# Kernel optimization log

Hardware: AMD Instinct MI355X
Metric: run time of the kernel (lower is better)

## Reference

```python
import jax, jax.numpy as jnp
import numpy as np

KH = KW = 3
STRIDE = 1
PAD = 1
DIL = 1


def _bilinear_sample(img, py, px):
    Hin, Win = img.shape[-2], img.shape[-1]
    y0 = jnp.floor(py)
    x0 = jnp.floor(px)
    y0i = y0.astype(jnp.int32)
    x0i = x0.astype(jnp.int32)
    wy = py - y0
    wx = px - x0

    def get(yi, xi):
        valid = (yi >= 0) & (yi < Hin) & (xi >= 0) & (xi < Win)
        yc = jnp.clip(yi, 0, Hin - 1)
        xc = jnp.clip(xi, 0, Win - 1)
        v = img[:, yc, xc]  # [C, K, H, W]
        return v * valid[None].astype(img.dtype)

    v00 = get(y0i, x0i)
    v01 = get(y0i, x0i + 1)
    v10 = get(y0i + 1, x0i)
    v11 = get(y0i + 1, x0i + 1)
    return (v00 * (1 - wy) * (1 - wx) + v01 * (1 - wy) * wx
            + v10 * wy * (1 - wx) + v11 * wy * wx)  # [C, K, H, W]


def _deform_conv(input, offset, mask, weight, bias):
    B, C, H, W = input.shape
    outH = (H + 2 * PAD - DIL * (KH - 1) - 1) // STRIDE + 1
    outW = (W + 2 * PAD - DIL * (KW - 1) - 1) // STRIDE + 1
    K = KH * KW
    # NOTE: DepthOffset in the original source overwrites its computed
    # depth-guided offsets with zeros and detaches them, so the effective
    # sampling offset is just `offset` (standard modulated deform conv, DCNv2).
    off = offset.reshape(B, K, 2, outH, outW)
    off_y = off[:, :, 0]  # [B, K, outH, outW]
    off_x = off[:, :, 1]
    ky = (jnp.arange(K) // KW) * DIL  # kernel-tap row offsets
    kx = (jnp.arange(K) % KW) * DIL
    ys = jnp.arange(outH) * STRIDE - PAD
    xs = jnp.arange(outW) * STRIDE - PAD
    base_y = (ky[:, None, None] + ys[None, :, None]).astype(input.dtype)  # [K, outH, 1]
    base_x = (kx[:, None, None] + xs[None, None, :]).astype(input.dtype)  # [K, 1, outW]
    py = base_y[None] + off_y  # [B, K, outH, outW]
    px = base_x[None] + off_x
    cols = jax.vmap(_bilinear_sample)(input, py, px)  # [B, C, K, outH, outW]
    cols = cols * mask[:, None]  # modulate by mask [B, 1, K, outH, outW]
    out = jnp.einsum('bckhw,ock->bohw', cols, weight.reshape(weight.shape[0], C, K))
    return out + bias[None, :, None, None]


def setup_inputs() -> dict:
    key = jax.random.key(0)
    ks = jax.random.split(key, 6)
    B, C, H, W = 4, 64, 128, 128
    O = 64
    fan_in = C * KH * KW
    bound = 1.0 / np.sqrt(fan_in)
    return {
        'input': jax.random.normal(ks[0], (B, C, H, W), dtype=jnp.float32),
        'depth': jax.random.uniform(ks[1], (B, 1, H, W), dtype=jnp.float32),
        'offset': jax.random.normal(ks[2], (B, 18, H, W), dtype=jnp.float32),
        'mask': jax.random.uniform(ks[3], (B, 9, H, W), dtype=jnp.float32),
        'weight': jax.random.uniform(ks[4], (O, C, KH, KW), dtype=jnp.float32,
                                     minval=-bound, maxval=bound),
        'bias': jax.random.uniform(ks[5], (O,), dtype=jnp.float32,
                                   minval=-bound, maxval=bound),
    }


def reference(input, depth, offset, mask, weight, bias):
    # depth-guided offsets are computed then zeroed+detached in the original
    # module, so depth does not influence the output.
    return _deform_conv(input, offset, mask, weight, bias)
```

## Files before the change

### kernel.cpp

```cpp
#include <hip/hip_runtime.h>


typedef __attribute__((ext_vector_type(8))) short bf16x8;
typedef __attribute__((ext_vector_type(4))) float f32x4;
typedef __attribute__((ext_vector_type(2))) float f32x2;
typedef __attribute__((ext_vector_type(4))) unsigned int u32x4;

#define HH 128
#define WW 128
#define CC 64
#define OO 64
#define HW (128 * 128)

__device__ __forceinline__ unsigned f32_to_bf16_rne(float f) {
    unsigned u = __float_as_uint(f);
    return (u + 0x7FFFu + ((u >> 16) & 1u)) >> 16;
}

__global__ __launch_bounds__(256)
void prep_fused15(const float* __restrict__ input,
                  unsigned short* __restrict__ nhwc,
                  const float* __restrict__ weight,
                  unsigned short* __restrict__ wT2)
{
    __shared__ unsigned tile[64][33];
    const int tid = threadIdx.x;
    const int blk = blockIdx.x;

    if (blk >= 2048) {
        const int d  = (blk - 2048) * 256 + tid;
        const int o  = d & 63;
        const int k8 = d >> 6;
        const int kt = k8 >> 3;
        const int c8 = k8 & 7;
        u32x4 pk;
        #pragma unroll
        for (int jj = 0; jj < 4; ++jj) {
            unsigned lo = f32_to_bf16_rne(weight[o * 576 + (c8 * 8 + 2 * jj)     * 9 + kt]);
            unsigned hi = f32_to_bf16_rne(weight[o * 576 + (c8 * 8 + 2 * jj + 1) * 9 + kt]);
            pk[jj] = lo | (hi << 16);
        }
        *(u32x4*)(wT2 + (size_t)d * 8) = pk;
        return;
    }

    const int b  = blk >> 9;
    const int y  = (blk >> 2) & 127;
    const int xbase = (blk & 3) * 32;
    #pragma unroll
    for (int it = 0; it < 2; ++it) {
        int flat = it * 256 + tid;
        int c = flat >> 3, x4 = flat & 7;
        const f32x4 v = *(const f32x4*)(input + ((b * 64 + c) * 128 + y) * 128 + xbase + x4 * 4);
        tile[c][x4 * 4 + 0] = f32_to_bf16_rne(v[0]);
        tile[c][x4 * 4 + 1] = f32_to_bf16_rne(v[1]);
        tile[c][x4 * 4 + 2] = f32_to_bf16_rne(v[2]);
        tile[c][x4 * 4 + 3] = f32_to_bf16_rne(v[3]);
    }
    __syncthreads();
    {
        int x = tid >> 3, cg = tid & 7;
        unsigned r0 = tile[cg * 8 + 0][x], r1 = tile[cg * 8 + 1][x];
        unsigned r2 = tile[cg * 8 + 2][x], r3 = tile[cg * 8 + 3][x];
        unsigned r4 = tile[cg * 8 + 4][x], r5 = tile[cg * 8 + 5][x];
        unsigned r6 = tile[cg * 8 + 6][x], r7 = tile[cg * 8 + 7][x];
        u32x4 pk;
        pk[0] = r0 | (r1 << 16); pk[1] = r2 | (r3 << 16);
        pk[2] = r4 | (r5 << 16); pk[3] = r6 | (r7 << 16);
        *(u32x4*)(nhwc + ((size_t)((b * 128 + y) * 128 + xbase + x)) * 64 + cg * 8) = pk;
    }
}

__global__ __launch_bounds__(1024)
void ddc_slim15(const unsigned short* __restrict__ nhwc,
                const unsigned short* __restrict__ wT2,
                const float* __restrict__ offset,
                const float* __restrict__ mask,
                const float* __restrict__ bias,
                float* __restrict__ out)
{
    __shared__ u32x4 win[8192];
    __shared__ float sten[6912];

    const int blk0 = blockIdx.x;
    const int blk  = (blk0 & 7) * 32 + (blk0 >> 3);
    const int b    = blk >> 6;
    const int h0   = (blk & 63) * 2;
    const int ys   = h0 - 3;
    const int tid  = threadIdx.x;
    const int wave = tid >> 6;
    const int lane = tid & 63;
    const int l15  = lane & 15;
    const int kq   = lane >> 4;
    const int hr   = wave >> 3;
    const int h    = h0 + hr;
    const int wpix = (wave & 7) * 16 + l15;

    f32x4 acc[4];
    #pragma unroll
    for (int mt = 0; mt < 4; ++mt) acc[mt] = (f32x4){0.f, 0.f, 0.f, 0.f};

    const unsigned short* nb = nhwc + (size_t)b * HW * CC;
    const u32x4* wsrc = (const u32x4*)wT2;

    #pragma unroll
    for (int it = 0; it < 7; ++it) {
        const int f = it * 1024 + tid;
        if (f < 6912) {
            const int plane = f >> 8;
            const int fr    = (f >> 7) & 1;
            const int x     = f & 127;
            sten[f] = (plane < 18)
                ? offset[((b * 18 + plane)      * 128 + (h0 + fr)) * 128 + x]
                : mask  [((b * 9 + (plane - 18))* 128 + (h0 + fr)) * 128 + x];
        }
    }

    #pragma unroll
    for (int slot = 0; slot < 8; ++slot) {
        const int y = ys + slot;
        if (y >= 0 && y < HH) {
            const int q  = tid;
            const int x  = q >> 3;
            const int c8 = q & 7;
            win[slot * 1024 + q] =
                *(const u32x4*)(nb + ((size_t)(y * WW + x)) * CC + ((c8 ^ (x & 7)) << 3));
        }
    }
    __syncthreads();

    #pragma unroll
    for (int kt = 0; kt < 9; ++kt) {
        const float oy = sten[(2 * kt)     * 256 + hr * 128 + wpix];
        const float ox = sten[(2 * kt + 1) * 256 + hr * 128 + wpix];
        const float m  = sten[(18 + kt)    * 256 + hr * 128 + wpix];

        const float py = (float)(h - 1 + kt / 3) + oy;
        const float px = (float)(wpix - 1 + kt % 3) + ox;
        const float y0f = floorf(py), x0f = floorf(px);
        const int y0 = (int)y0f, x0 = (int)x0f;
        const float wy = py - y0f, wx = px - x0f;
        const int y1 = y0 + 1, x1 = x0 + 1;
        const bool vy0 = (y0 >= 0) & (y0 < HH);
        const bool vy1 = (y1 >= 0) & (y1 < HH);
        const bool vx0 = (x0 >= 0) & (x0 < WW);
        const bool vx1 = (x1 >= 0) & (x1 < WW);
        const int y0c = min(max(y0, 0), HH - 1), y1c = min(max(y1, 0), HH - 1);
        const int x0c = min(max(x0, 0), WW - 1), x1c = min(max(x1, 0), WW - 1);
        const float wy1 = 1.f - wy, wx1 = 1.f - wx;
        const float c00 = (vy0 && vx0) ? wy1 * wx1 * m : 0.f;
        const float c01 = (vy0 && vx1) ? wy1 * wx  * m : 0.f;
        const float c10 = (vy1 && vx0) ? wy  * wx1 * m : 0.f;
        const float c11 = (vy1 && vx1) ? wy  * wx  * m : 0.f;

        const int s0 = y0c - ys, s1 = y1c - ys;
        const bool in0 = ((unsigned)s0 < 8u);
        const bool in1 = ((unsigned)s1 < 8u);
        const int r0 = (in0 ? s0 : 0) * 1024;
        const int r1 = (in1 ? s1 : 0) * 1024;
        const int bx0 = x0c * 8, sx0 = x0c & 7;
        const int bx1 = x1c * 8, sx1 = x1c & 7;

        const f32x2 vc00 = (f32x2){c00, c00}, vc01 = (f32x2){c01, c01};
        const f32x2 vc10 = (f32x2){c10, c10}, vc11 = (f32x2){c11, c11};

        #pragma unroll
        for (int ks = 0; ks < 2; ++ks) {
            const int ch = ks * 4 + kq;

            u32x4 w00 = win[r0 + bx0 + (ch ^ sx0)];
            u32x4 w01 = win[r0 + bx1 + (ch ^ sx1)];
            u32x4 w10 = win[r1 + bx0 + (ch ^ sx0)];
            u32x4 w11 = win[r1 + bx1 + (ch ^ sx1)];
            if (!in0) {
                w00 = *(const u32x4*)(nb + ((size_t)y0c * WW + x0c) * CC + ch * 8);
                w01 = *(const u32x4*)(nb + ((size_t)y0c * WW + x1c) * CC + ch * 8);
            }
            if (!in1) {
                w10 = *(const u32x4*)(nb + ((size_t)y1c * WW + x0c) * CC + ch * 8);
                w11 = *(const u32x4*)(nb + ((size_t)y1c * WW + x1c) * CC + ch * 8);
            }

            u32x4 pk;
            #pragma unroll
            for (int j = 0; j < 4; ++j) {
                const f32x2 A = (f32x2){__uint_as_float(w00[j] << 16),
                                        __uint_as_float(w00[j] & 0xFFFF0000u)};
                const f32x2 B = (f32x2){__uint_as_float(w01[j] << 16),
                                        __uint_as_float(w01[j] & 0xFFFF0000u)};
                const f32x2 D = (f32x2){__uint_as_float(w10[j] << 16),
                                        __uint_as_float(w10[j] & 0xFFFF0000u)};
                const f32x2 E = (f32x2){__uint_as_float(w11[j] << 16),
                                        __uint_as_float(w11[j] & 0xFFFF0000u)};
                const f32x2 S = vc00 * A + vc01 * B + vc10 * D + vc11 * E;
                unsigned r;
                asm("v_cvt_pk_bf16_f32 %0, %1, %2" : "=v"(r) : "v"(S[0]), "v"(S[1]));
                pk[j] = r;
            }
            const bf16x8 bfrag = __builtin_bit_cast(bf16x8, pk);

            const u32x4* wp = wsrc + (kt * 8 + ks * 4 + kq) * 64 + l15;
            acc[0] = __builtin_amdgcn_mfma_f32_16x16x32_bf16(
                __builtin_bit_cast(bf16x8, wp[0]),  bfrag, acc[0], 0, 0, 0);
            acc[1] = __builtin_amdgcn_mfma_f32_16x16x32_bf16(
                __builtin_bit_cast(bf16x8, wp[16]), bfrag, acc[1], 0, 0, 0);
            acc[2] = __builtin_amdgcn_mfma_f32_16x16x32_bf16(
                __builtin_bit_cast(bf16x8, wp[32]), bfrag, acc[2], 0, 0, 0);
            acc[3] = __builtin_amdgcn_mfma_f32_16x16x32_bf16(
                __builtin_bit_cast(bf16x8, wp[48]), bfrag, acc[3], 0, 0, 0);
        }
    }

    #pragma unroll
    for (int mt = 0; mt < 4; ++mt) {
        const f32x4 bv = *(const f32x4*)(bias + mt * 16 + kq * 4);
        #pragma unroll
        for (int r = 0; r < 4; ++r) {
            const int o = mt * 16 + kq * 4 + r;
            out[((b * 64 + o) * 128 + h) * 128 + wpix] = acc[mt][r] + bv[r];
        }
    }
}

extern "C" void kernel_launch(void* const* d_in, const int* in_sizes, int n_in,
                              void* d_out, int out_size, void* d_ws, size_t ws_size,
                              hipStream_t stream)
{
    const float* input  = (const float*)d_in[0];
    const float* offset = (const float*)d_in[2];
    const float* mask   = (const float*)d_in[3];
    const float* weight = (const float*)d_in[4];
    const float* bias   = (const float*)d_in[5];
    float* out = (float*)d_out;

    unsigned short* nhwc = (unsigned short*)d_ws;
    unsigned short* wT2  = nhwc + (size_t)4 * HW * CC;

    prep_fused15<<<dim3(2066), dim3(256), 0, stream>>>(input, nhwc, weight, wT2);
    ddc_slim15<<<dim3(256), dim3(1024), 0, stream>>>(nhwc, wT2, offset, mask, bias, out);
}
```

Before: 104.6 us.

## Fuse prep and deform-conv kernels with a grid-wide atomic barrier

Merges the bf16 NHWC transpose and weight repacking into the main deformable-conv kernel. Each of the 256 blocks converts two input rows, and the first few blocks also repack the weights. A global atomic-counter spin barrier then waits for all blocks before the gather and MFMA phase. This removes one kernel launch and the gap between the two kernels, but it relies on all 256 blocks being co-resident and adds a memset plus the barrier spin. It also reuses the shared window buffer as the transpose tile.

Result: slower. 148.6 us (+42.0%).

```diff
diff --git a/kernel.cpp b/kernel.cpp
--- a/kernel.cpp
+++ b/kernel.cpp
@@ -17,77 +17,75 @@
     return (u + 0x7FFFu + ((u >> 16) & 1u)) >> 16;
 }
 
-__global__ __launch_bounds__(256)
-void prep_fused15(const float* __restrict__ input,
-                  unsigned short* __restrict__ nhwc,
-                  const float* __restrict__ weight,
-                  unsigned short* __restrict__ wT2)
-{
-    __shared__ unsigned tile[64][33];
-    const int tid = threadIdx.x;
-    const int blk = blockIdx.x;
-
-    if (blk >= 2048) {
-        const int d  = (blk - 2048) * 256 + tid;
-        const int o  = d & 63;
-        const int k8 = d >> 6;
-        const int kt = k8 >> 3;
-        const int c8 = k8 & 7;
-        u32x4 pk;
-        #pragma unroll
-        for (int jj = 0; jj < 4; ++jj) {
-            unsigned lo = f32_to_bf16_rne(weight[o * 576 + (c8 * 8 + 2 * jj)     * 9 + kt]);
-            unsigned hi = f32_to_bf16_rne(weight[o * 576 + (c8 * 8 + 2 * jj + 1) * 9 + kt]);
-            pk[jj] = lo | (hi << 16);
-        }
-        *(u32x4*)(wT2 + (size_t)d * 8) = pk;
-        return;
-    }
-
-    const int b  = blk >> 9;
-    const int y  = (blk >> 2) & 127;
-    const int xbase = (blk & 3) * 32;
-    #pragma unroll
-    for (int it = 0; it < 2; ++it) {
-        int flat = it * 256 + tid;
-        int c = flat >> 3, x4 = flat & 7;
-        const f32x4 v = *(const f32x4*)(input + ((b * 64 + c) * 128 + y) * 128 + xbase + x4 * 4);
-        tile[c][x4 * 4 + 0] = f32_to_bf16_rne(v[0]);
-        tile[c][x4 * 4 + 1] = f32_to_bf16_rne(v[1]);
-        tile[c][x4 * 4 + 2] = f32_to_bf16_rne(v[2]);
-        tile[c][x4 * 4 + 3] = f32_to_bf16_rne(v[3]);
-    }
-    __syncthreads();
-    {
-        int x = tid >> 3, cg = tid & 7;
-        unsigned r0 = tile[cg * 8 + 0][x], r1 = tile[cg * 8 + 1][x];
-        unsigned r2 = tile[cg * 8 + 2][x], r3 = tile[cg * 8 + 3][x];
-        unsigned r4 = tile[cg * 8 + 4][x], r5 = tile[cg * 8 + 5][x];
-        unsigned r6 = tile[cg * 8 + 6][x], r7 = tile[cg * 8 + 7][x];
-        u32x4 pk;
-        pk[0] = r0 | (r1 << 16); pk[1] = r2 | (r3 << 16);
-        pk[2] = r4 | (r5 << 16); pk[3] = r6 | (r7 << 16);
-        *(u32x4*)(nhwc + ((size_t)((b * 128 + y) * 128 + xbase + x)) * 64 + cg * 8) = pk;
-    }
-}
-
 __global__ __launch_bounds__(1024)
-void ddc_slim15(const unsigned short* __restrict__ nhwc,
-                const unsigned short* __restrict__ wT2,
-                const float* __restrict__ offset,
-                const float* __restrict__ mask,
-                const float* __restrict__ bias,
-                float* __restrict__ out)
+void ddc_fused16(const float* __restrict__ input,
+                 unsigned short* __restrict__ nhwc,
+                 const float* __restrict__ weight,
+                 unsigned short* __restrict__ wT2,
+                 const float* __restrict__ offset,
+                 const float* __restrict__ mask,
+                 const float* __restrict__ bias,
+                 float* __restrict__ out,
+                 int* __restrict__ flag)
 {
     __shared__ u32x4 win[8192];
     __shared__ float sten[6912];
 
     const int blk0 = blockIdx.x;
+    const int tid  = threadIdx.x;
+
+    {
+        unsigned (*tile)[129] = (unsigned (*)[129])win;
+        #pragma unroll
+        for (int rr = 0; rr < 2; ++rr) {
+            const int r = blk0 * 2 + rr;
+            const int pb = r >> 7, py = r & 127;
+            #pragma unroll
+            for (int it = 0; it < 2; ++it) {
+                const int f = it * 1024 + tid;
+                const int c = f >> 5, x4 = f & 31;
+                const f32x4 v = *(const f32x4*)(input + ((pb * 64 + c) * 128 + py) * 128 + x4 * 4);
+                tile[c][x4 * 4 + 0] = f32_to_bf16_rne(v[0]);
+                tile[c][x4 * 4 + 1] = f32_to_bf16_rne(v[1]);
+                tile[c][x4 * 4 + 2] = f32_to_bf16_rne(v[2]);
+                tile[c][x4 * 4 + 3] = f32_to_bf16_rne(v[3]);
+            }
+            __syncthreads();
+            {
+                const int x = tid >> 3, cg = tid & 7;
+                unsigned r0 = tile[cg * 8 + 0][x], r1 = tile[cg * 8 + 1][x];
+                unsigned r2 = tile[cg * 8 + 2][x], r3 = tile[cg * 8 + 3][x];
+                unsigned r4 = tile[cg * 8 + 4][x], r5 = tile[cg * 8 + 5][x];
+                unsigned r6 = tile[cg * 8 + 6][x], r7 = tile[cg * 8 + 7][x];
+                u32x4 pk;
+                pk[0] = r0 | (r1 << 16); pk[1] = r2 | (r3 << 16);
+                pk[2] = r4 | (r5 << 16); pk[3] = r6 | (r7 << 16);
+                *(u32x4*)(nhwc + ((size_t)((pb * 128 + py) * 128 + x)) * 64 + cg * 8) = pk;
+            }
+            __syncthreads();
+        }
+        const int d = blk0 * 1024 + tid;
+        if (d < 4608) {
+            const int o  = d & 63;
+            const int k8 = d >> 6;
+            const int kt = k8 >> 3;
+            const int c8 = k8 & 7;
+            u32x4 pk;
+            #pragma unroll
+            for (int jj = 0; jj < 4; ++jj) {
+                unsigned lo = f32_to_bf16_rne(weight[o * 576 + (c8 * 8 + 2 * jj)     * 9 + kt]);
+                unsigned hi = f32_to_bf16_rne(weight[o * 576 + (c8 * 8 + 2 * jj + 1) * 9 + kt]);
+                pk[jj] = lo | (hi << 16);
+            }
+            *(u32x4*)(wT2 + (size_t)d * 8) = pk;
+        }
+        __syncthreads();
+    }
+
     const int blk  = (blk0 & 7) * 32 + (blk0 >> 3);
     const int b    = blk >> 6;
     const int h0   = (blk & 63) * 2;
     const int ys   = h0 - 3;
-    const int tid  = threadIdx.x;
     const int wave = tid >> 6;
     const int lane = tid & 63;
     const int l15  = lane & 15;
@@ -95,13 +93,6 @@
     const int hr   = wave >> 3;
     const int h    = h0 + hr;
     const int wpix = (wave & 7) * 16 + l15;
-
-    f32x4 acc[4];
-    #pragma unroll
-    for (int mt = 0; mt < 4; ++mt) acc[mt] = (f32x4){0.f, 0.f, 0.f, 0.f};
-
-    const unsigned short* nb = nhwc + (size_t)b * HW * CC;
-    const u32x4* wsrc = (const u32x4*)wT2;
 
     #pragma unroll
     for (int it = 0; it < 7; ++it) {
@@ -115,6 +106,24 @@
                 : mask  [((b * 9 + (plane - 18))* 128 + (h0 + fr)) * 128 + x];
         }
     }
+
+    if (tid == 0) {
+        __hip_atomic_fetch_add(flag, 1, __ATOMIC_RELEASE, __HIP_MEMORY_SCOPE_AGENT);
+        int spins = 0;
+        while (__hip_atomic_load(flag, __ATOMIC_ACQUIRE, __HIP_MEMORY_SCOPE_AGENT) < 256
+               && spins < (1 << 27)) {
+            __builtin_amdgcn_s_sleep(8);
+            ++spins;
+        }
+    }
+    __syncthreads();
+
+    f32x4 acc[4];
+    #pragma unroll
+    for (int mt = 0; mt < 4; ++mt) acc[mt] = (f32x4){0.f, 0.f, 0.f, 0.f};
+
+    const unsigned short* nb = nhwc + (size_t)b * HW * CC;
+    const u32x4* wsrc = (const u32x4*)wT2;
 
     #pragma unroll
     for (int slot = 0; slot < 8; ++slot) {
@@ -235,7 +244,9 @@
 
     unsigned short* nhwc = (unsigned short*)d_ws;
     unsigned short* wT2  = nhwc + (size_t)4 * HW * CC;
-
-    prep_fused15<<<dim3(2066), dim3(256), 0, stream>>>(input, nhwc, weight, wT2);
-    ddc_slim15<<<dim3(256), dim3(1024), 0, stream>>>(nhwc, wT2, offset, mask, bias, out);
+    int* flag = (int*)((char*)d_ws + (16u << 20));
+
+    hipMemsetAsync(flag, 0, 4, stream);
+    ddc_fused16<<<dim3(256), dim3(1024), 0, stream>>>(
+        input, nhwc, weight, wT2, offset, mask, bias, out, flag);
 }
```

## Fuse NCHW-to-bf16 NHWC conversion into deform conv kernel window load

Applied to the files above, without the earlier changes.

Drops the separate prep pass that wrote a bf16 NHWC copy of the input. The main kernel now reads fp32 NCHW rows directly, converts them to bf16 and transposes them through a shared-memory tile into the swizzled window. Out-of-window samples read fp32 from global memory and convert on the fly. This removes a full-tensor write and re-read plus part of a launch, at the cost of extra barriers and serialized per-row staging inside the main kernel. It also raises wave priority around the MFMA block with s_setprio.

Result: slower. 110.7 us (+5.8%).

```diff
diff --git a/kernel.cpp b/kernel.cpp
--- a/kernel.cpp
+++ b/kernel.cpp
@@ -4,6 +4,7 @@
 typedef __attribute__((ext_vector_type(8))) short bf16x8;
 typedef __attribute__((ext_vector_type(4))) float f32x4;
 typedef __attribute__((ext_vector_type(2))) float f32x2;
+typedef __attribute__((ext_vector_type(2))) unsigned int u32x2;
 typedef __attribute__((ext_vector_type(4))) unsigned int u32x4;
 
 #define HH 128
@@ -17,70 +18,41 @@
     return (u + 0x7FFFu + ((u >> 16) & 1u)) >> 16;
 }
 
+__device__ __forceinline__ unsigned cvtpk_bf16(float lo, float hi) {
+    unsigned r;
+    asm("v_cvt_pk_bf16_f32 %0, %1, %2" : "=v"(r) : "v"(lo), "v"(hi));
+    return r;
+}
+
 __global__ __launch_bounds__(256)
-void prep_fused15(const float* __restrict__ input,
-                  unsigned short* __restrict__ nhwc,
-                  const float* __restrict__ weight,
-                  unsigned short* __restrict__ wT2)
+void prep_w17(const float* __restrict__ weight,
+              unsigned short* __restrict__ wT2)
 {
-    __shared__ unsigned tile[64][33];
-    const int tid = threadIdx.x;
-    const int blk = blockIdx.x;
-
-    if (blk >= 2048) {
-        const int d  = (blk - 2048) * 256 + tid;
-        const int o  = d & 63;
-        const int k8 = d >> 6;
-        const int kt = k8 >> 3;
-        const int c8 = k8 & 7;
-        u32x4 pk;
-        #pragma unroll
-        for (int jj = 0; jj < 4; ++jj) {
-            unsigned lo = f32_to_bf16_rne(weight[o * 576 + (c8 * 8 + 2 * jj)     * 9 + kt]);
-            unsigned hi = f32_to_bf16_rne(weight[o * 576 + (c8 * 8 + 2 * jj + 1) * 9 + kt]);
-            pk[jj] = lo | (hi << 16);
-        }
-        *(u32x4*)(wT2 + (size_t)d * 8) = pk;
-        return;
-    }
-
-    const int b  = blk >> 9;
-    const int y  = (blk >> 2) & 127;
-    const int xbase = (blk & 3) * 32;
-    #pragma unroll
-    for (int it = 0; it < 2; ++it) {
-        int flat = it * 256 + tid;
-        int c = flat >> 3, x4 = flat & 7;
-        const f32x4 v = *(const f32x4*)(input + ((b * 64 + c) * 128 + y) * 128 + xbase + x4 * 4);
-        tile[c][x4 * 4 + 0] = f32_to_bf16_rne(v[0]);
-        tile[c][x4 * 4 + 1] = f32_to_bf16_rne(v[1]);
-        tile[c][x4 * 4 + 2] = f32_to_bf16_rne(v[2]);
-        tile[c][x4 * 4 + 3] = f32_to_bf16_rne(v[3]);
-    }
-    __syncthreads();
-    {
-        int x = tid >> 3, cg = tid & 7;
-        unsigned r0 = tile[cg * 8 + 0][x], r1 = tile[cg * 8 + 1][x];
-        unsigned r2 = tile[cg * 8 + 2][x], r3 = tile[cg * 8 + 3][x];
-        unsigned r4 = tile[cg * 8 + 4][x], r5 = tile[cg * 8 + 5][x];
-        unsigned r6 = tile[cg * 8 + 6][x], r7 = tile[cg * 8 + 7][x];
-        u32x4 pk;
-        pk[0] = r0 | (r1 << 16); pk[1] = r2 | (r3 << 16);
-        pk[2] = r4 | (r5 << 16); pk[3] = r6 | (r7 << 16);
-        *(u32x4*)(nhwc + ((size_t)((b * 128 + y) * 128 + xbase + x)) * 64 + cg * 8) = pk;
-    }
+    const int d  = blockIdx.x * 256 + threadIdx.x;
+    const int o  = d & 63;
+    const int k8 = d >> 6;
+    const int kt = k8 >> 3;
+    const int c8 = k8 & 7;
+    u32x4 pk;
+    #pragma unroll
+    for (int jj = 0; jj < 4; ++jj) {
+        unsigned lo = f32_to_bf16_rne(weight[o * 576 + (c8 * 8 + 2 * jj)     * 9 + kt]);
+        unsigned hi = f32_to_bf16_rne(weight[o * 576 + (c8 * 8 + 2 * jj + 1) * 9 + kt]);
+        pk[jj] = lo | (hi << 16);
+    }
+    *(u32x4*)(wT2 + (size_t)d * 8) = pk;
 }
 
 __global__ __launch_bounds__(1024)
-void ddc_slim15(const unsigned short* __restrict__ nhwc,
-                const unsigned short* __restrict__ wT2,
-                const float* __restrict__ offset,
-                const float* __restrict__ mask,
-                const float* __restrict__ bias,
-                float* __restrict__ out)
+void ddc_inline17(const float* __restrict__ input,
+                  const unsigned short* __restrict__ wT2,
+                  const float* __restrict__ offset,
+                  const float* __restrict__ mask,
+                  const float* __restrict__ bias,
+                  float* __restrict__ out)
 {
     __shared__ u32x4 win[8192];
-    __shared__ float sten[6912];
+    __shared__ unsigned scratch[6912];
 
     const int blk0 = blockIdx.x;
     const int blk  = (blk0 & 7) * 32 + (blk0 >> 3);
@@ -96,13 +68,43 @@
     const int h    = h0 + hr;
     const int wpix = (wave & 7) * 16 + l15;
 
-    f32x4 acc[4];
-    #pragma unroll
-    for (int mt = 0; mt < 4; ++mt) acc[mt] = (f32x4){0.f, 0.f, 0.f, 0.f};
-
-    const unsigned short* nb = nhwc + (size_t)b * HW * CC;
-    const u32x4* wsrc = (const u32x4*)wT2;
-
+    const float* ib = input + (size_t)b * 64 * HW;
+
+    unsigned (*tileN)[66] = (unsigned (*)[66])scratch;
+    #pragma unroll 1
+    for (int slot = 0; slot < 8; ++slot) {
+        const int y = ys + slot;
+        const bool yok = (y >= 0) & (y < HH);
+        if (yok) {
+            #pragma unroll
+            for (int it = 0; it < 2; ++it) {
+                const int f  = it * 1024 + tid;
+                const int c  = f >> 5, x4 = f & 31;
+                const f32x4 v = *(const f32x4*)(ib + ((size_t)c * 128 + y) * 128 + x4 * 4);
+                u32x2 w;
+                w[0] = cvtpk_bf16(v[0], v[1]);
+                w[1] = cvtpk_bf16(v[2], v[3]);
+                *(u32x2*)&tileN[c][x4 * 2] = w;
+            }
+        }
+        __syncthreads();
+        if (yok) {
+            const int x  = tid >> 3;
+            const int c8 = tid & 7;
+            const int xw = x >> 1, sh = (x & 1) * 16;
+            u32x4 pk;
+            #pragma unroll
+            for (int j = 0; j < 4; ++j) {
+                const unsigned lo = (tileN[c8 * 8 + 2 * j    ][xw] >> sh) & 0xFFFFu;
+                const unsigned hi = (tileN[c8 * 8 + 2 * j + 1][xw] >> sh) & 0xFFFFu;
+                pk[j] = lo | (hi << 16);
+            }
+            win[slot * 1024 + x * 8 + (c8 ^ (x & 7))] = pk;
+        }
+        __syncthreads();
+    }
+
+    float* sten = (float*)scratch;
     #pragma unroll
     for (int it = 0; it < 7; ++it) {
         const int f = it * 1024 + tid;
@@ -115,19 +117,13 @@
                 : mask  [((b * 9 + (plane - 18))* 128 + (h0 + fr)) * 128 + x];
         }
     }
-
-    #pragma unroll
-    for (int slot = 0; slot < 8; ++slot) {
-        const int y = ys + slot;
-        if (y >= 0 && y < HH) {
-            const int q  = tid;
-            const int x  = q >> 3;
-            const int c8 = q & 7;
-            win[slot * 1024 + q] =
-                *(const u32x4*)(nb + ((size_t)(y * WW + x)) * CC + ((c8 ^ (x & 7)) << 3));
-        }
-    }
     __syncthreads();
+
+    f32x4 acc[4];
+    #pragma unroll
+    for (int mt = 0; mt < 4; ++mt) acc[mt] = (f32x4){0.f, 0.f, 0.f, 0.f};
+
+    const u32x4* wsrc = (const u32x4*)wT2;
 
     #pragma unroll
     for (int kt = 0; kt < 9; ++kt) {
@@ -173,12 +169,20 @@
             u32x4 w10 = win[r1 + bx0 + (ch ^ sx0)];
             u32x4 w11 = win[r1 + bx1 + (ch ^ sx1)];
             if (!in0) {
-                w00 = *(const u32x4*)(nb + ((size_t)y0c * WW + x0c) * CC + ch * 8);
-                w01 = *(const u32x4*)(nb + ((size_t)y0c * WW + x1c) * CC + ch * 8);
+                const float* p = ib + (size_t)ch * 8 * HW + (size_t)y0c * WW;
+                #pragma unroll
+                for (int j = 0; j < 4; ++j) {
+                    w00[j] = cvtpk_bf16(p[(2*j)*HW + x0c], p[(2*j+1)*HW + x0c]);
+                    w01[j] = cvtpk_bf16(p[(2*j)*HW + x1c], p[(2*j+1)*HW + x1c]);
+                }
             }
             if (!in1) {
-                w10 = *(const u32x4*)(nb + ((size_t)y1c * WW + x0c) * CC + ch * 8);
-                w11 = *(const u32x4*)(nb + ((size_t)y1c * WW + x1c) * CC + ch * 8);
+                const float* p = ib + (size_t)ch * 8 * HW + (size_t)y1c * WW;
+                #pragma unroll
+                for (int j = 0; j < 4; ++j) {
+                    w10[j] = cvtpk_bf16(p[(2*j)*HW + x0c], p[(2*j+1)*HW + x0c]);
+                    w11[j] = cvtpk_bf16(p[(2*j)*HW + x1c], p[(2*j+1)*HW + x1c]);
+                }
             }
 
             u32x4 pk;
@@ -193,13 +197,12 @@
                 const f32x2 E = (f32x2){__uint_as_float(w11[j] << 16),
                                         __uint_as_float(w11[j] & 0xFFFF0000u)};
                 const f32x2 S = vc00 * A + vc01 * B + vc10 * D + vc11 * E;
-                unsigned r;
-                asm("v_cvt_pk_bf16_f32 %0, %1, %2" : "=v"(r) : "v"(S[0]), "v"(S[1]));
-                pk[j] = r;
+                pk[j] = cvtpk_bf16(S[0], S[1]);
             }
             const bf16x8 bfrag = __builtin_bit_cast(bf16x8, pk);
 
             const u32x4* wp = wsrc + (kt * 8 + ks * 4 + kq) * 64 + l15;
+            __builtin_amdgcn_s_setprio(1);
             acc[0] = __builtin_amdgcn_mfma_f32_16x16x32_bf16(
                 __builtin_bit_cast(bf16x8, wp[0]),  bfrag, acc[0], 0, 0, 0);
             acc[1] = __builtin_amdgcn_mfma_f32_16x16x32_bf16(
@@ -208,6 +211,7 @@
                 __builtin_bit_cast(bf16x8, wp[32]), bfrag, acc[2], 0, 0, 0);
             acc[3] = __builtin_amdgcn_mfma_f32_16x16x32_bf16(
                 __builtin_bit_cast(bf16x8, wp[48]), bfrag, acc[3], 0, 0, 0);
+            __builtin_amdgcn_s_setprio(0);
         }
     }
 
@@ -233,9 +237,9 @@
     const float* bias   = (const float*)d_in[5];
     float* out = (float*)d_out;
 
-    unsigned short* nhwc = (unsigned short*)d_ws;
-    unsigned short* wT2  = nhwc + (size_t)4 * HW * CC;
-
-    prep_fused15<<<dim3(2066), dim3(256), 0, stream>>>(input, nhwc, weight, wT2);
-    ddc_slim15<<<dim3(256), dim3(1024), 0, stream>>>(nhwc, wT2, offset, mask, bias, out);
-}
+    unsigned short* wT2 = (unsigned short*)d_ws;
+
+    prep_w17<<<dim3(18), dim3(256), 0, stream>>>(weight, wT2);
+    ddc_inline17<<<dim3(256), dim3(1024), 0, stream>>>(
+        input, wT2, offset, mask, bias, out);
+}
```

## Split kernel taps across waves, drop LDS window, gather directly from global

Applied to the files above, without the earlier changes.

Replaces the 2-row, 1024-thread block that staged an 8-row NHWC window in LDS with a 512-thread block per half row. The 9 kernel taps are split across two wave groups (5 and 4 taps), whose partial accumulators are merged through a small padded shared buffer before the bias add and store. Bilinear corner values are now gathered straight from global/L2 instead of the LDS window, which shrinks LDS use and should raise occupancy and block count. The cost is more global gather traffic, an extra sync and merge step, and uneven work between the two wave groups.

Result: slower. 128.7 us (+23.0%).

```diff
diff --git a/kernel.cpp b/kernel.cpp
--- a/kernel.cpp
+++ b/kernel.cpp
@@ -17,8 +17,14 @@
     return (u + 0x7FFFu + ((u >> 16) & 1u)) >> 16;
 }
 
+__device__ __forceinline__ unsigned cvtpk_bf16(float lo, float hi) {
+    unsigned r;
+    asm("v_cvt_pk_bf16_f32 %0, %1, %2" : "=v"(r) : "v"(lo), "v"(hi));
+    return r;
+}
+
 __global__ __launch_bounds__(256)
-void prep_fused15(const float* __restrict__ input,
+void prep_fused20(const float* __restrict__ input,
                   unsigned short* __restrict__ nhwc,
                   const float* __restrict__ weight,
                   unsigned short* __restrict__ wT2)
@@ -71,30 +77,31 @@
     }
 }
 
-__global__ __launch_bounds__(1024)
-void ddc_slim15(const unsigned short* __restrict__ nhwc,
-                const unsigned short* __restrict__ wT2,
-                const float* __restrict__ offset,
-                const float* __restrict__ mask,
-                const float* __restrict__ bias,
-                float* __restrict__ out)
+__global__ __launch_bounds__(512, 8)
+void ddc_split20(const unsigned short* __restrict__ nhwc,
+                 const unsigned short* __restrict__ wT2,
+                 const float* __restrict__ offset,
+                 const float* __restrict__ mask,
+                 const float* __restrict__ bias,
+                 float* __restrict__ out)
 {
-    __shared__ u32x4 win[8192];
-    __shared__ float sten[6912];
+    __shared__ float sten[1728];
+    __shared__ float mrg[4352];
 
     const int blk0 = blockIdx.x;
-    const int blk  = (blk0 & 7) * 32 + (blk0 >> 3);
-    const int b    = blk >> 6;
-    const int h0   = (blk & 63) * 2;
-    const int ys   = h0 - 3;
+    const int blk  = (blk0 & 7) * 128 + (blk0 >> 3);
+    const int b    = blk >> 8;
+    const int h    = (blk >> 1) & 127;
+    const int wh   = blk & 1;
     const int tid  = threadIdx.x;
     const int wave = tid >> 6;
     const int lane = tid & 63;
     const int l15  = lane & 15;
     const int kq   = lane >> 4;
-    const int hr   = wave >> 3;
-    const int h    = h0 + hr;
-    const int wpix = (wave & 7) * 16 + l15;
+    const int pxg  = wave & 3;
+    const int kh   = wave >> 2;
+    const int pxl  = pxg * 16 + l15;
+    const int wpix = wh * 64 + pxl;
 
     f32x4 acc[4];
     #pragma unroll
@@ -104,120 +111,116 @@
     const u32x4* wsrc = (const u32x4*)wT2;
 
     #pragma unroll
-    for (int it = 0; it < 7; ++it) {
-        const int f = it * 1024 + tid;
-        if (f < 6912) {
-            const int plane = f >> 8;
-            const int fr    = (f >> 7) & 1;
-            const int x     = f & 127;
+    for (int it = 0; it < 4; ++it) {
+        const int f = it * 512 + tid;
+        if (f < 1728) {
+            const int plane = f >> 6;
+            const int x     = f & 63;
             sten[f] = (plane < 18)
-                ? offset[((b * 18 + plane)      * 128 + (h0 + fr)) * 128 + x]
-                : mask  [((b * 9 + (plane - 18))* 128 + (h0 + fr)) * 128 + x];
-        }
-    }
-
-    #pragma unroll
-    for (int slot = 0; slot < 8; ++slot) {
-        const int y = ys + slot;
-        if (y >= 0 && y < HH) {
-            const int q  = tid;
-            const int x  = q >> 3;
-            const int c8 = q & 7;
-            win[slot * 1024 + q] =
-                *(const u32x4*)(nb + ((size_t)(y * WW + x)) * CC + ((c8 ^ (x & 7)) << 3));
+                ? offset[((b * 18 + plane)       * 128 + h) * 128 + wh * 64 + x]
+                : mask  [((b * 9 + (plane - 18)) * 128 + h) * 128 + wh * 64 + x];
         }
     }
     __syncthreads();
 
-    #pragma unroll
-    for (int kt = 0; kt < 9; ++kt) {
-        const float oy = sten[(2 * kt)     * 256 + hr * 128 + wpix];
-        const float ox = sten[(2 * kt + 1) * 256 + hr * 128 + wpix];
-        const float m  = sten[(18 + kt)    * 256 + hr * 128 + wpix];
-
-        const float py = (float)(h - 1 + kt / 3) + oy;
-        const float px = (float)(wpix - 1 + kt % 3) + ox;
-        const float y0f = floorf(py), x0f = floorf(px);
-        const int y0 = (int)y0f, x0 = (int)x0f;
-        const float wy = py - y0f, wx = px - x0f;
-        const int y1 = y0 + 1, x1 = x0 + 1;
-        const bool vy0 = (y0 >= 0) & (y0 < HH);
-        const bool vy1 = (y1 >= 0) & (y1 < HH);
-        const bool vx0 = (x0 >= 0) & (x0 < WW);
-        const bool vx1 = (x1 >= 0) & (x1 < WW);
-        const int y0c = min(max(y0, 0), HH - 1), y1c = min(max(y1, 0), HH - 1);
-        const int x0c = min(max(x0, 0), WW - 1), x1c = min(max(x1, 0), WW - 1);
-        const float wy1 = 1.f - wy, wx1 = 1.f - wx;
-        const float c00 = (vy0 && vx0) ? wy1 * wx1 * m : 0.f;
-        const float c01 = (vy0 && vx1) ? wy1 * wx  * m : 0.f;
-        const float c10 = (vy1 && vx0) ? wy  * wx1 * m : 0.f;
-        const float c11 = (vy1 && vx1) ? wy  * wx  * m : 0.f;
-
-        const int s0 = y0c - ys, s1 = y1c - ys;
-        const bool in0 = ((unsigned)s0 < 8u);
-        const bool in1 = ((unsigned)s1 < 8u);
-        const int r0 = (in0 ? s0 : 0) * 1024;
-        const int r1 = (in1 ? s1 : 0) * 1024;
-        const int bx0 = x0c * 8, sx0 = x0c & 7;
-        const int bx1 = x1c * 8, sx1 = x1c & 7;
-
-        const f32x2 vc00 = (f32x2){c00, c00}, vc01 = (f32x2){c01, c01};
-        const f32x2 vc10 = (f32x2){c10, c10}, vc11 = (f32x2){c11, c11};
-
+    const int kt0 = kh ? 5 : 0;
+    const int nkt = kh ? 4 : 5;
+    #pragma unroll
+    for (int i = 0; i < 5; ++i) {
+        if (i < nkt) {
+            const int kt = kt0 + i;
+            const int ky = (kt * 11) >> 5;
+            const int kx = kt - ky * 3;
+
+            const float oy = sten[(2 * kt)     * 64 + pxl];
+            const float ox = sten[(2 * kt + 1) * 64 + pxl];
+            const float m  = sten[(18 + kt)    * 64 + pxl];
+
+            const float py = (float)(h - 1 + ky) + oy;
+            const float px = (float)(wpix - 1 + kx) + ox;
+            const float y0f = floorf(py), x0f = floorf(px);
+            const int y0 = (int)y0f, x0 = (int)x0f;
+            const float wy = py - y0f, wx = px - x0f;
+            const int y1 = y0 + 1, x1 = x0 + 1;
+            const bool vy0 = (y0 >= 0) & (y0 < HH);
+            const bool vy1 = (y1 >= 0) & (y1 < HH);
+            const bool vx0 = (x0 >= 0) & (x0 < WW);
+            const bool vx1 = (x1 >= 0) & (x1 < WW);
+            const int y0c = min(max(y0, 0), HH - 1), y1c = min(max(y1, 0), HH - 1);
+            const int x0c = min(max(x0, 0), WW - 1), x1c = min(max(x1, 0), WW - 1);
+            const float wy1 = 1.f - wy, wx1 = 1.f - wx;
+            const float c00 = (vy0 && vx0) ? wy1 * wx1 * m : 0.f;
+            const float c01 = (vy0 && vx1) ? wy1 * wx  * m : 0.f;
+            const float c10 = (vy1 && vx0) ? wy  * wx1 * m : 0.f;
+            const float c11 = (vy1 && vx1) ? wy  * wx  * m : 0.f;
+
+            const f32x2 vc00 = (f32x2){c00, c00}, vc01 = (f32x2){c01, c01};
+            const f32x2 vc10 = (f32x2){c10, c10}, vc11 = (f32x2){c11, c11};
+
+            const unsigned short* p00 = nb + ((size_t)y0c * WW + x0c) * CC;
+            const unsigned short* p01 = nb + ((size_t)y0c * WW + x1c) * CC;
+            const unsigned short* p10 = nb + ((size_t)y1c * WW + x0c) * CC;
+            const unsigned short* p11 = nb + ((size_t)y1c * WW + x1c) * CC;
+
+            #pragma unroll
+            for (int ks = 0; ks < 2; ++ks) {
+                const int co = (ks * 4 + kq) * 8;
+
+                const u32x4 w00 = *(const u32x4*)(p00 + co);
+                const u32x4 w01 = *(const u32x4*)(p01 + co);
+                const u32x4 w10 = *(const u32x4*)(p10 + co);
+                const u32x4 w11 = *(const u32x4*)(p11 + co);
+
+                u32x4 pk;
+                #pragma unroll
+                for (int j = 0; j < 4; ++j) {
+                    const f32x2 A = (f32x2){__uint_as_float(w00[j] << 16),
+                                            __uint_as_float(w00[j] & 0xFFFF0000u)};
+                    const f32x2 B = (f32x2){__uint_as_float(w01[j] << 16),
+                                            __uint_as_float(w01[j] & 0xFFFF0000u)};
+                    const f32x2 D = (f32x2){__uint_as_float(w10[j] << 16),
+                                            __uint_as_float(w10[j] & 0xFFFF0000u)};
+                    const f32x2 E = (f32x2){__uint_as_float(w11[j] << 16),
+                                            __uint_as_float(w11[j] & 0xFFFF0000u)};
+                    const f32x2 S = vc00 * A + vc01 * B + vc10 * D + vc11 * E;
+                    pk[j] = cvtpk_bf16(S[0], S[1]);
+                }
+                const bf16x8 bfrag = __builtin_bit_cast(bf16x8, pk);
+
+                const u32x4* wp = wsrc + (kt * 8 + ks * 4 + kq) * 64 + l15;
+                acc[0] = __builtin_amdgcn_mfma_f32_16x16x32_bf16(
+                    __builtin_bit_cast(bf16x8, wp[0]),  bfrag, acc[0], 0, 0, 0);
+                acc[1] = __builtin_amdgcn_mfma_f32_16x16x32_bf16(
+                    __builtin_bit_cast(bf16x8, wp[16]), bfrag, acc[1], 0, 0, 0);
+                acc[2] = __builtin_amdgcn_mfma_f32_16x16x32_bf16(
+                    __builtin_bit_cast(bf16x8, wp[32]), bfrag, acc[2], 0, 0, 0);
+                acc[3] = __builtin_amdgcn_mfma_f32_16x16x32_bf16(
+                    __builtin_bit_cast(bf16x8, wp[48]), bfrag, acc[3], 0, 0, 0);
+            }
+        }
+    }
+
+    if (kh) {
         #pragma unroll
-        for (int ks = 0; ks < 2; ++ks) {
-            const int ch = ks * 4 + kq;
-
-            u32x4 w00 = win[r0 + bx0 + (ch ^ sx0)];
-            u32x4 w01 = win[r0 + bx1 + (ch ^ sx1)];
-            u32x4 w10 = win[r1 + bx0 + (ch ^ sx0)];
-            u32x4 w11 = win[r1 + bx1 + (ch ^ sx1)];
-            if (!in0) {
-                w00 = *(const u32x4*)(nb + ((size_t)y0c * WW + x0c) * CC + ch * 8);
-                w01 = *(const u32x4*)(nb + ((size_t)y0c * WW + x1c) * CC + ch * 8);
+        for (int mt = 0; mt < 4; ++mt) {
+            #pragma unroll
+            for (int r = 0; r < 4; ++r) {
+                const int o = mt * 16 + kq * 4 + r;
+                mrg[(pxg * 64 + o) * 17 + l15] = acc[mt][r];
             }
-            if (!in1) {
-                w10 = *(const u32x4*)(nb + ((size_t)y1c * WW + x0c) * CC + ch * 8);
-                w11 = *(const u32x4*)(nb + ((size_t)y1c * WW + x1c) * CC + ch * 8);
+        }
+    }
+    __syncthreads();
+    if (!kh) {
+        #pragma unroll
+        for (int mt = 0; mt < 4; ++mt) {
+            const f32x4 bv = *(const f32x4*)(bias + mt * 16 + kq * 4);
+            #pragma unroll
+            for (int r = 0; r < 4; ++r) {
+                const int o = mt * 16 + kq * 4 + r;
+                out[((b * 64 + o) * 128 + h) * 128 + wpix] =
+                    acc[mt][r] + mrg[(pxg * 64 + o) * 17 + l15] + bv[r];
             }
-
-            u32x4 pk;
-            #pragma unroll
-            for (int j = 0; j < 4; ++j) {
-                const f32x2 A = (f32x2){__uint_as_float(w00[j] << 16),
-                                        __uint_as_float(w00[j] & 0xFFFF0000u)};
-                const f32x2 B = (f32x2){__uint_as_float(w01[j] << 16),
-                                        __uint_as_float(w01[j] & 0xFFFF0000u)};
-                const f32x2 D = (f32x2){__uint_as_float(w10[j] << 16),
-                                        __uint_as_float(w10[j] & 0xFFFF0000u)};
-                const f32x2 E = (f32x2){__uint_as_float(w11[j] << 16),
-                                        __uint_as_float(w11[j] & 0xFFFF0000u)};
-                const f32x2 S = vc00 * A + vc01 * B + vc10 * D + vc11 * E;
-                unsigned r;
-                asm("v_cvt_pk_bf16_f32 %0, %1, %2" : "=v"(r) : "v"(S[0]), "v"(S[1]));
-                pk[j] = r;
-            }
-            const bf16x8 bfrag = __builtin_bit_cast(bf16x8, pk);
-
-            const u32x4* wp = wsrc + (kt * 8 + ks * 4 + kq) * 64 + l15;
-            acc[0] = __builtin_amdgcn_mfma_f32_16x16x32_bf16(
-                __builtin_bit_cast(bf16x8, wp[0]),  bfrag, acc[0], 0, 0, 0);
-            acc[1] = __builtin_amdgcn_mfma_f32_16x16x32_bf16(
-                __builtin_bit_cast(bf16x8, wp[16]), bfrag, acc[1], 0, 0, 0);
-            acc[2] = __builtin_amdgcn_mfma_f32_16x16x32_bf16(
-                __builtin_bit_cast(bf16x8, wp[32]), bfrag, acc[2], 0, 0, 0);
-            acc[3] = __builtin_amdgcn_mfma_f32_16x16x32_bf16(
-                __builtin_bit_cast(bf16x8, wp[48]), bfrag, acc[3], 0, 0, 0);
-        }
-    }
-
-    #pragma unroll
-    for (int mt = 0; mt < 4; ++mt) {
-        const f32x4 bv = *(const f32x4*)(bias + mt * 16 + kq * 4);
-        #pragma unroll
-        for (int r = 0; r < 4; ++r) {
-            const int o = mt * 16 + kq * 4 + r;
-            out[((b * 64 + o) * 128 + h) * 128 + wpix] = acc[mt][r] + bv[r];
         }
     }
 }
@@ -236,6 +239,6 @@
     unsigned short* nhwc = (unsigned short*)d_ws;
     unsigned short* wT2  = nhwc + (size_t)4 * HW * CC;
 
-    prep_fused15<<<dim3(2066), dim3(256), 0, stream>>>(input, nhwc, weight, wT2);
-    ddc_slim15<<<dim3(256), dim3(1024), 0, stream>>>(nhwc, wT2, offset, mask, bias, out);
-}
+    prep_fused20<<<dim3(2066), dim3(256), 0, stream>>>(input, nhwc, weight, wT2);
+    ddc_split20<<<dim3(1024), dim3(512), 0, stream>>>(nhwc, wT2, offset, mask, bias, out);
+}
```
